# Optimization experiments

Hardware: AMD Instinct MI355X
Metric: run time of the kernel (lower is better)

Reference implementation:

```python
import jax, jax.numpy as jnp
import numpy as np

B, C, N, K, OUT = 8, 64, 40962, 7, 64

def setup_inputs() -> dict:
    key = jax.random.key(0)
    k1, k2, k3, k4 = jax.random.split(key, 4)
    x = jax.random.normal(k1, (B, C, N), dtype=jnp.float32)
    neigh_orders = jax.random.randint(k2, (K * N,), 0, N, dtype=jnp.int64)
    # nn.Linear(7*C, OUT): W [OUT, 7*C], b [OUT]
    W = jax.random.normal(k3, (OUT, K * C), dtype=jnp.float32) * (1.0 / np.sqrt(K * C))
    b = jax.random.normal(k4, (OUT,), dtype=jnp.float32) * 0.01
    return {"x": x, "neigh_orders": neigh_orders, "W": W, "b": b}

def reference(x, neigh_orders, W, b):
    Bn, Cn, Nn = x.shape
    # gather 7-ring neighborhood: [B, C, N*7] -> [B, C, N, 7]
    mat = x[:, :, neigh_orders].reshape(Bn, Cn, Nn, K)
    # torch flattens (7, C) with 7 outer after permute -> W reshaped to [OUT, 7, C]
    W3 = W.reshape(W.shape[0], K, Cn)
    # fused gather-GEMM: [B,C,N,7] x [O,7,C] -> [B,O,N]
    out = jnp.einsum('bcnk,okc->bon', mat, W3) + b[None, :, None]
    return out
```

## Files before the change

kernel.cpp:

```cpp
#include <hip/hip_runtime.h>
#include <hip/hip_bf16.h>

#define Bn   8
#define Cn   64
#define Nn   40962
#define Kn   7
#define OUTn 64

typedef __bf16 bf16x8 __attribute__((ext_vector_type(8)));
typedef __bf16 bf16x4 __attribute__((ext_vector_type(4)));
typedef float  f32x4  __attribute__((ext_vector_type(4)));

__global__ __launch_bounds__(256) void convw_kernel(
    const float* __restrict__ W, __bf16* __restrict__ Wb)
{
    int i = blockIdx.x * 256 + threadIdx.x;
    if (i < OUTn * Kn * Cn) Wb[i] = (__bf16)W[i];
}

__global__ __launch_bounds__(256) void transpose_kernel(
    const float* __restrict__ x, __bf16* __restrict__ xT, int b0)
{
    __shared__ unsigned int tile[64][65];
    const int tid  = threadIdx.x;
    const int lane = tid & 63;
    const int w    = tid >> 6;
    const int n0   = blockIdx.x * 128;
    const int bl   = blockIdx.y;
    const int b    = b0 + bl;
    const size_t xb = (size_t)b * Cn * Nn;

    const int n = n0 + lane * 2;
    if (n < Nn) {
#pragma unroll
        for (int i = 0; i < 16; ++i) {
            const int c = w * 16 + i;
            const float2 v = *(const float2*)(x + xb + (size_t)c * Nn + n);
            const unsigned short ua =
                __builtin_bit_cast(unsigned short, (__bf16)v.x);
            const unsigned short ub =
                __builtin_bit_cast(unsigned short, (__bf16)v.y);
            tile[c][lane] = ((unsigned)ub << 16) | (unsigned)ua;
        }
    }
    __syncthreads();

    const int rsub = lane >> 3;
    const int cblk = lane & 7;
#pragma unroll
    for (int it = 0; it < 4; ++it) {
        const int row = it * 32 + w * 8 + rsub;
        const int n1  = n0 + row;
        if (n1 < Nn) {
            const int slot = row >> 1;
            const int sh   = (row & 1) * 16;
            bf16x8 frag;
#pragma unroll
            for (int e = 0; e < 8; ++e) {
                const unsigned u = tile[cblk * 8 + e][slot];
                frag[e] = __builtin_bit_cast(
                    __bf16, (unsigned short)((u >> sh) & 0xffffu));
            }
            *(bf16x8*)(xT + ((size_t)bl * Nn + n1) * Cn + cblk * 8) = frag;
        }
    }
}

__global__ __launch_bounds__(256) void gconv_kernel(
    const __bf16* __restrict__ xT,
    const int*    __restrict__ nbr,
    const __bf16* __restrict__ Wb,
    const float*  __restrict__ bias,
    float*        __restrict__ out,
    int b0, int curB)
{
    __shared__ __bf16 buf[2][64][64];

    const int bl    = blockIdx.x % curB;
    const int vtile = blockIdx.x / curB;
    const int w     = threadIdx.x >> 6;
    const int l     = threadIdx.x & 63;
    const int col   = l & 15;
    const int quad  = l >> 4;
    const int b     = b0 + bl;
    const int v0    = vtile * 64;

    const __bf16* xb = xT + (size_t)bl * Nn * Cn;

    bf16x8 aW[14];
#pragma unroll
    for (int kc = 0; kc < 14; ++kc)
        aW[kc] = *(const bf16x8*)(Wb + (size_t)(w * 16 + col) * (Kn * Cn)
                                     + kc * 32 + quad * 8);

    const int rme = l >> 3;
    int ofs[2][7];
#pragma unroll
    for (int j = 0; j < 2; ++j) {
        int v = v0 + w * 16 + j * 8 + rme;
        if (v > Nn - 1) v = Nn - 1;
#pragma unroll
        for (int kn = 0; kn < 7; ++kn) {
            int id = nbr[v * 7 + kn];
            id = id < 0 ? 0 : (id >= Nn ? Nn - 1 : id);
            ofs[j][kn] = id * (Cn * 2);
        }
    }
    const int srcoff = ((l & 7) ^ rme) * 16;

#define STAGE(p_, kn_)                                                        \
    {                                                                         \
        _Pragma("unroll")                                                     \
        for (int j = 0; j < 2; ++j) {                                         \
            const char* src_ = (const char*)xb + ofs[j][kn_] + srcoff;        \
            __builtin_amdgcn_global_load_lds(                                 \
                (const unsigned int*)src_,                                    \
                (unsigned int*)&buf[p_][w * 16 + j * 8][0], 16, 0, 0);        \
        }                                                                     \
    }

    f32x4 acc[4];
#pragma unroll
    for (int t = 0; t < 4; ++t)
        acc[t] = (f32x4){0.f, 0.f, 0.f, 0.f};

    STAGE(0, 0)
    __syncthreads();

#pragma unroll
    for (int kn = 0; kn < 7; ++kn) {
        if (kn < 6) STAGE((kn + 1) & 1, kn + 1)
        const int p = kn & 1;
#pragma unroll
        for (int h = 0; h < 2; ++h) {
            const int kc = kn * 2 + h;
            const int q  = h * 4 + quad;
#pragma unroll
            for (int t = 0; t < 4; ++t) {
                const int r    = t * 16 + col;
                const int slot = q ^ (r & 7);
                const bf16x8 bf = *(const bf16x8*)&buf[p][r][slot * 8];
                acc[t] = __builtin_amdgcn_mfma_f32_16x16x32_bf16(
                    aW[kc], bf, acc[t], 0, 0, 0);
            }
        }
        __syncthreads();
    }
#undef STAGE

#pragma unroll
    for (int r4 = 0; r4 < 4; ++r4) {
        const int o  = w * 16 + quad * 4 + r4;
        const float bv = bias[o];
#pragma unroll
        for (int t = 0; t < 4; ++t) {
            const int n = v0 + t * 16 + col;
            if (n < Nn)
                out[((size_t)b * OUTn + o) * Nn + n] = acc[t][r4] + bv;
        }
    }
}

__global__ __launch_bounds__(256) void naive_kernel(
    const float* __restrict__ x,
    const int*   __restrict__ nbr,
    const float* __restrict__ W,
    const float* __restrict__ bias,
    float*       __restrict__ out)
{
    __shared__ float xs[4][Kn * Cn];
    const int v = threadIdx.x >> 6;
    const int o = threadIdx.x & 63;
    const int b = blockIdx.y;
    const int n = blockIdx.x * 4 + v;
    const bool ok = n < Nn;
    const int nn = ok ? n : 0;

#pragma unroll
    for (int k = 0; k < Kn; ++k) {
        int id = nbr[nn * Kn + k];
        id = id < 0 ? 0 : (id >= Nn ? Nn - 1 : id);
        xs[v][k * Cn + o] = x[((size_t)b * Cn + o) * Nn + id];
    }
    __syncthreads();

    float acc = bias[o];
    for (int j = 0; j < Kn * Cn; ++j)
        acc += W[o * (Kn * Cn) + j] * xs[v][j];

    if (ok)
        out[((size_t)b * OUTn + o) * Nn + n] = acc;
}

extern "C" void kernel_launch(void* const* d_in, const int* in_sizes, int n_in,
                              void* d_out, int out_size, void* d_ws, size_t ws_size,
                              hipStream_t stream)
{
    const float* x    = (const float*)d_in[0];
    const int*   nbr  = (const int*)d_in[1];
    const float* W    = (const float*)d_in[2];
    const float* bias = (const float*)d_in[3];
    float*       out  = (float*)d_out;

    const size_t w_bytes     = (size_t)OUTn * Kn * Cn * sizeof(__bf16);
    const size_t batch_bytes = (size_t)Nn * Cn * sizeof(__bf16);
    int nb = 0;
    if (ws_size > w_bytes)
        nb = (int)((ws_size - w_bytes) / batch_bytes);
    if (nb > Bn) nb = Bn;

    if (nb >= 1) {
        __bf16* Wb = (__bf16*)d_ws;
        __bf16* xT = (__bf16*)((char*)d_ws + w_bytes);

        convw_kernel<<<(OUTn * Kn * Cn + 255) / 256, 256, 0, stream>>>(W, Wb);

        const int vtiles = (Nn + 63) / 64;
        for (int b0 = 0; b0 < Bn; b0 += nb) {
            int cur = (Bn - b0) < nb ? (Bn - b0) : nb;
            dim3 tgrid((Nn + 127) / 128, cur);
            transpose_kernel<<<tgrid, 256, 0, stream>>>(x, xT, b0);
            gconv_kernel<<<vtiles * cur, 256, 0, stream>>>(xT, nbr, Wb, bias, out, b0, cur);
        }
    } else {
        dim3 ngrid((Nn + 3) / 4, Bn);
        naive_kernel<<<ngrid, 256, 0, stream>>>(x, nbr, W, bias, out);
    }
}
```

Baseline: 225.7 us.

## Deepen gather pipeline to four LDS buffers and fold weight conversion into transpose

The gather-GEMM kernel now uses four LDS buffers and issues three neighbor stages ahead. Each step waits with explicit vmcnt counts followed by a bare barrier, replacing the full __syncthreads after every step. MFMA sections run at raised wave priority. The bf16 weight conversion moves into the transpose kernel's first-batch blocks, which removes one kernel launch. The change doubles LDS per block, which may lower occupancy, and the weights are now reconverted on every batch-chunk iteration.

```diff
diff --git a/kernel.cpp b/kernel.cpp
--- a/kernel.cpp
+++ b/kernel.cpp
@@ -11,15 +11,9 @@
 typedef __bf16 bf16x4 __attribute__((ext_vector_type(4)));
 typedef float  f32x4  __attribute__((ext_vector_type(4)));
 
-__global__ __launch_bounds__(256) void convw_kernel(
-    const float* __restrict__ W, __bf16* __restrict__ Wb)
-{
-    int i = blockIdx.x * 256 + threadIdx.x;
-    if (i < OUTn * Kn * Cn) Wb[i] = (__bf16)W[i];
-}
-
 __global__ __launch_bounds__(256) void transpose_kernel(
-    const float* __restrict__ x, __bf16* __restrict__ xT, int b0)
+    const float* __restrict__ x, __bf16* __restrict__ xT,
+    const float* __restrict__ W, __bf16* __restrict__ Wb, int b0)
 {
     __shared__ unsigned int tile[64][65];
     const int tid  = threadIdx.x;
@@ -30,6 +24,11 @@
     const int b    = b0 + bl;
     const size_t xb = (size_t)b * Cn * Nn;
 
+    if (bl == 0) {
+        const int wi = blockIdx.x * 256 + tid;
+        if (wi < OUTn * Kn * Cn) Wb[wi] = (__bf16)W[wi];
+    }
+
     const int n = n0 + lane * 2;
     if (n < Nn) {
 #pragma unroll
@@ -74,7 +73,7 @@
     float*        __restrict__ out,
     int b0, int curB)
 {
-    __shared__ __bf16 buf[2][64][64];
+    __shared__ __bf16 buf[4][64][64];
 
     const int bl    = blockIdx.x % curB;
     const int vtile = blockIdx.x / curB;
@@ -119,33 +118,50 @@
         }                                                                     \
     }
 
+#define WAITVM_(n_) asm volatile("s_waitcnt vmcnt(" #n_ ")" ::: "memory")
+#define WAITVM(n_) WAITVM_(n_)
+
     f32x4 acc[4];
 #pragma unroll
     for (int t = 0; t < 4; ++t)
         acc[t] = (f32x4){0.f, 0.f, 0.f, 0.f};
 
     STAGE(0, 0)
-    __syncthreads();
-
-#pragma unroll
-    for (int kn = 0; kn < 7; ++kn) {
-        if (kn < 6) STAGE((kn + 1) & 1, kn + 1)
-        const int p = kn & 1;
-#pragma unroll
-        for (int h = 0; h < 2; ++h) {
-            const int kc = kn * 2 + h;
-            const int q  = h * 4 + quad;
-#pragma unroll
-            for (int t = 0; t < 4; ++t) {
-                const int r    = t * 16 + col;
-                const int slot = q ^ (r & 7);
-                const bf16x8 bf = *(const bf16x8*)&buf[p][r][slot * 8];
-                acc[t] = __builtin_amdgcn_mfma_f32_16x16x32_bf16(
-                    aW[kc], bf, acc[t], 0, 0, 0);
-            }
-        }
-        __syncthreads();
-    }
+    STAGE(1, 1)
+    STAGE(2, 2)
+
+#define KNSTEP(kn_, vm_)                                                      \
+    {                                                                         \
+        WAITVM(vm_);                             \
+        __builtin_amdgcn_s_barrier();            \
+        __builtin_amdgcn_sched_barrier(0);                                    \
+        if ((kn_) + 3 < 7) STAGE(((kn_) + 3) & 3, (kn_) + 3)                  \
+        __builtin_amdgcn_s_setprio(1);                                        \
+        _Pragma("unroll")                                                     \
+        for (int h = 0; h < 2; ++h) {                      \
+            const int q = h * 4 + quad;          \
+            _Pragma("unroll")                                                 \
+            for (int t = 0; t < 4; ++t) {                                     \
+                const int r    = t * 16 + col;                                \
+                const int slot = q ^ (r & 7);                                 \
+                const bf16x8 bf =                                             \
+                    *(const bf16x8*)&buf[(kn_) & 3][r][slot * 8];             \
+                acc[t] = __builtin_amdgcn_mfma_f32_16x16x32_bf16(             \
+                    aW[(kn_)*2 + h], bf, acc[t], 0, 0, 0);                    \
+            }                                                                 \
+        }                                                                     \
+        __builtin_amdgcn_s_setprio(0);                                        \
+    }
+
+    KNSTEP(0, 4)
+    KNSTEP(1, 4)
+    KNSTEP(2, 4)
+    KNSTEP(3, 4)
+    KNSTEP(4, 4)
+    KNSTEP(5, 2)
+    KNSTEP(6, 0)
+
+#undef KNSTEP
 #undef STAGE
 
 #pragma unroll
@@ -213,13 +229,11 @@
         __bf16* Wb = (__bf16*)d_ws;
         __bf16* xT = (__bf16*)((char*)d_ws + w_bytes);
 
-        convw_kernel<<<(OUTn * Kn * Cn + 255) / 256, 256, 0, stream>>>(W, Wb);
-
         const int vtiles = (Nn + 63) / 64;
         for (int b0 = 0; b0 < Bn; b0 += nb) {
             int cur = (Bn - b0) < nb ? (Bn - b0) : nb;
             dim3 tgrid((Nn + 127) / 128, cur);
-            transpose_kernel<<<tgrid, 256, 0, stream>>>(x, xT, b0);
+            transpose_kernel<<<tgrid, 256, 0, stream>>>(x, xT, W, Wb, b0);
             gconv_kernel<<<vtiles * cur, 256, 0, stream>>>(xT, nbr, Wb, bias, out, b0, cur);
         }
     } else {
```

Measured after the change: 221.8 us. No clear change (-1.7%).

## Make gather-GEMM kernel persistent with all-neighbor staging and fused weight conversion

Applied to the files above, without the earlier changes.

Turns the gconv kernel into a persistent grid of 512 blocks, each looping over vertex tiles for one batch. Weights stay in registers across tiles, and the next tile's neighbor indices are prefetched while the current one computes. All 7 neighbor slices are staged into LDS at once, replacing the double-buffered per-neighbor pipeline. The weight-conversion kernel is folded into the transpose kernel to save a launch, and the batch-chunk path is dropped, so the fast path now needs workspace for all 8 batches and otherwise falls back to the naive kernel. The larger LDS footprint (56KB) and fewer syncs per tile trade occupancy for less per-tile setup.

```diff
diff --git a/kernel.cpp b/kernel.cpp
--- a/kernel.cpp
+++ b/kernel.cpp
@@ -6,20 +6,15 @@
 #define Nn   40962
 #define Kn   7
 #define OUTn 64
+#define NVT  641
 
 typedef __bf16 bf16x8 __attribute__((ext_vector_type(8)));
 typedef __bf16 bf16x4 __attribute__((ext_vector_type(4)));
 typedef float  f32x4  __attribute__((ext_vector_type(4)));
 
-__global__ __launch_bounds__(256) void convw_kernel(
-    const float* __restrict__ W, __bf16* __restrict__ Wb)
-{
-    int i = blockIdx.x * 256 + threadIdx.x;
-    if (i < OUTn * Kn * Cn) Wb[i] = (__bf16)W[i];
-}
-
 __global__ __launch_bounds__(256) void transpose_kernel(
-    const float* __restrict__ x, __bf16* __restrict__ xT, int b0)
+    const float* __restrict__ x, __bf16* __restrict__ xT,
+    const float* __restrict__ W, __bf16* __restrict__ Wb, int b0)
 {
     __shared__ unsigned int tile[64][65];
     const int tid  = threadIdx.x;
@@ -30,6 +25,11 @@
     const int b    = b0 + bl;
     const size_t xb = (size_t)b * Cn * Nn;
 
+    if (bl == 0) {
+        const int wi = blockIdx.x * 256 + tid;
+        if (wi < OUTn * Kn * Cn) Wb[wi] = (__bf16)W[wi];
+    }
+
     const int n = n0 + lane * 2;
     if (n < Nn) {
 #pragma unroll
@@ -66,25 +66,24 @@
     }
 }
 
-__global__ __launch_bounds__(256) void gconv_kernel(
+__global__ __launch_bounds__(256, 2) void gconv_kernel(
     const __bf16* __restrict__ xT,
     const int*    __restrict__ nbr,
     const __bf16* __restrict__ Wb,
     const float*  __restrict__ bias,
-    float*        __restrict__ out,
-    int b0, int curB)
-{
-    __shared__ __bf16 buf[2][64][64];
-
-    const int bl    = blockIdx.x % curB;
-    const int vtile = blockIdx.x / curB;
-    const int w     = threadIdx.x >> 6;
-    const int l     = threadIdx.x & 63;
-    const int col   = l & 15;
-    const int quad  = l >> 4;
-    const int b     = b0 + bl;
-    const int v0    = vtile * 64;
-
+    float*        __restrict__ out)
+{
+    __shared__ __bf16 sbuf[Kn][64][64];
+
+    const int blk  = blockIdx.x;
+    const int bl   = blk & 7;
+    const int grp  = blk >> 3;
+    const int w    = threadIdx.x >> 6;
+    const int l    = threadIdx.x & 63;
+    const int col  = l & 15;
+    const int quad = l >> 4;
+    const int rme  = l >> 3;
+    const int srcoff = ((l & 7) ^ rme) * 16;
     const __bf16* xb = xT + (size_t)bl * Nn * Cn;
 
     bf16x8 aW[14];
@@ -93,80 +92,96 @@
         aW[kc] = *(const bf16x8*)(Wb + (size_t)(w * 16 + col) * (Kn * Cn)
                                      + kc * 32 + quad * 8);
 
-    const int rme = l >> 3;
-    int ofs[2][7];
-#pragma unroll
-    for (int j = 0; j < 2; ++j) {
-        int v = v0 + w * 16 + j * 8 + rme;
-        if (v > Nn - 1) v = Nn - 1;
-#pragma unroll
-        for (int kn = 0; kn < 7; ++kn) {
-            int id = nbr[v * 7 + kn];
-            id = id < 0 ? 0 : (id >= Nn ? Nn - 1 : id);
-            ofs[j][kn] = id * (Cn * 2);
-        }
-    }
-    const int srcoff = ((l & 7) ^ rme) * 16;
-
-#define STAGE(p_, kn_)                                                        \
+    const float bv[4] = {bias[w * 16 + quad * 4 + 0],
+                         bias[w * 16 + quad * 4 + 1],
+                         bias[w * 16 + quad * 4 + 2],
+                         bias[w * 16 + quad * 4 + 3]};
+
+#define LOADIDX(vt_, dst_)                                                    \
     {                                                                         \
         _Pragma("unroll")                                                     \
         for (int j = 0; j < 2; ++j) {                                         \
-            const char* src_ = (const char*)xb + ofs[j][kn_] + srcoff;        \
-            __builtin_amdgcn_global_load_lds(                                 \
-                (const unsigned int*)src_,                                    \
-                (unsigned int*)&buf[p_][w * 16 + j * 8][0], 16, 0, 0);        \
+            int v = (vt_)*64 + w * 16 + j * 8 + rme;                          \
+            if (v > Nn - 1) v = Nn - 1;                                       \
+            _Pragma("unroll")                                                 \
+            for (int kn = 0; kn < Kn; ++kn) {                                 \
+                int id = nbr[v * 7 + kn];                                     \
+                id = id < 0 ? 0 : (id >= Nn ? Nn - 1 : id);                   \
+                dst_[j][kn] = id * (Cn * 2);                                  \
+            }                                                                 \
         }                                                                     \
     }
 
-    f32x4 acc[4];
-#pragma unroll
-    for (int t = 0; t < 4; ++t)
-        acc[t] = (f32x4){0.f, 0.f, 0.f, 0.f};
-
-    STAGE(0, 0)
-    __syncthreads();
-
-#pragma unroll
-    for (int kn = 0; kn < 7; ++kn) {
-        if (kn < 6) STAGE((kn + 1) & 1, kn + 1)
-        const int p = kn & 1;
-#pragma unroll
-        for (int h = 0; h < 2; ++h) {
-            const int kc = kn * 2 + h;
-            const int q  = h * 4 + quad;
+    int ofsA[2][Kn];
+    LOADIDX(grp, ofsA)
+
+    for (int vt = grp; vt < NVT; vt += 64) {
+        __syncthreads();
+
+#pragma unroll
+        for (int kn = 0; kn < Kn; ++kn) {
+#pragma unroll
+            for (int j = 0; j < 2; ++j) {
+                const char* src_ = (const char*)xb + ofsA[j][kn] + srcoff;
+                __builtin_amdgcn_global_load_lds(
+                    (const unsigned int*)src_,
+                    (unsigned int*)&sbuf[kn][w * 16 + j * 8][0], 16, 0, 0);
+            }
+        }
+
+        int ofsB[2][Kn];
+        LOADIDX(vt + 64, ofsB)
+
+        __syncthreads();
+
+        f32x4 acc[4];
+#pragma unroll
+        for (int t = 0; t < 4; ++t)
+            acc[t] = (f32x4){0.f, 0.f, 0.f, 0.f};
+
+        __builtin_amdgcn_s_setprio(1);
+#pragma unroll
+        for (int kn = 0; kn < Kn; ++kn) {
+#pragma unroll
+            for (int h = 0; h < 2; ++h) {
+                const int q = h * 4 + quad;
+#pragma unroll
+                for (int t = 0; t < 4; ++t) {
+                    const int r    = t * 16 + col;
+                    const int slot = q ^ (r & 7);
+                    const bf16x8 bf = *(const bf16x8*)&sbuf[kn][r][slot * 8];
+                    acc[t] = __builtin_amdgcn_mfma_f32_16x16x32_bf16(
+                        aW[kn * 2 + h], bf, acc[t], 0, 0, 0);
+                }
+            }
+        }
+        __builtin_amdgcn_s_setprio(0);
+
+        const int v0 = vt * 64;
+#pragma unroll
+        for (int r4 = 0; r4 < 4; ++r4) {
+            const int o = w * 16 + quad * 4 + r4;
 #pragma unroll
             for (int t = 0; t < 4; ++t) {
-                const int r    = t * 16 + col;
-                const int slot = q ^ (r & 7);
-                const bf16x8 bf = *(const bf16x8*)&buf[p][r][slot * 8];
-                acc[t] = __builtin_amdgcn_mfma_f32_16x16x32_bf16(
-                    aW[kc], bf, acc[t], 0, 0, 0);
-            }
-        }
-        __syncthreads();
-    }
-#undef STAGE
-
-#pragma unroll
-    for (int r4 = 0; r4 < 4; ++r4) {
-        const int o  = w * 16 + quad * 4 + r4;
-        const float bv = bias[o];
-#pragma unroll
-        for (int t = 0; t < 4; ++t) {
-            const int n = v0 + t * 16 + col;
-            if (n < Nn)
-                out[((size_t)b * OUTn + o) * Nn + n] = acc[t][r4] + bv;
-        }
-    }
+                const int n = v0 + t * 16 + col;
+                if (n < Nn)
+                    out[((size_t)bl * OUTn + o) * Nn + n] = acc[t][r4] + bv[r4];
+            }
+        }
+
+#pragma unroll
+        for (int j = 0; j < 2; ++j)
+#pragma unroll
+            for (int kn = 0; kn < Kn; ++kn)
+                ofsA[j][kn] = ofsB[j][kn];
+    }
+#undef LOADIDX
 }
 
 __global__ __launch_bounds__(256) void naive_kernel(
-    const float* __restrict__ x,
-    const int*   __restrict__ nbr,
-    const float* __restrict__ W,
-    const float* __restrict__ bias,
-    float*       __restrict__ out)
+    const float* __restrict__ x, const int* __restrict__ nbr,
+    const float* __restrict__ W, const float* __restrict__ bias,
+    float* __restrict__ out)
 {
     __shared__ float xs[4][Kn * Cn];
     const int v = threadIdx.x >> 6;
@@ -209,19 +224,13 @@
         nb = (int)((ws_size - w_bytes) / batch_bytes);
     if (nb > Bn) nb = Bn;
 
-    if (nb >= 1) {
+    if (nb >= Bn) {
         __bf16* Wb = (__bf16*)d_ws;
         __bf16* xT = (__bf16*)((char*)d_ws + w_bytes);
 
-        convw_kernel<<<(OUTn * Kn * Cn + 255) / 256, 256, 0, stream>>>(W, Wb);
-
-        const int vtiles = (Nn + 63) / 64;
-        for (int b0 = 0; b0 < Bn; b0 += nb) {
-            int cur = (Bn - b0) < nb ? (Bn - b0) : nb;
-            dim3 tgrid((Nn + 127) / 128, cur);
-            transpose_kernel<<<tgrid, 256, 0, stream>>>(x, xT, b0);
-            gconv_kernel<<<vtiles * cur, 256, 0, stream>>>(xT, nbr, Wb, bias, out, b0, cur);
-        }
+        dim3 tgrid((Nn + 127) / 128, Bn);
+        transpose_kernel<<<tgrid, 256, 0, stream>>>(x, xT, W, Wb, 0);
+        gconv_kernel<<<512, 256, 0, stream>>>(xT, nbr, Wb, bias, out);
     } else {
         dim3 ngrid((Nn + 3) / 4, Bn);
         naive_kernel<<<ngrid, 256, 0, stream>>>(x, nbr, W, bias, out);
```

Result: faster. 205.9 us (-8.8%).
